# Optimization experiments

Hardware: AMD Instinct MI355X
Metric: run time of the kernel (lower is better)

## Reference

```python
import math
import jax, jax.numpy as jnp
import numpy as np

B = 2
TMAX = 1024
D = 1024
H = 16
DK = D // H
F = 4096
L = 2
CHUNK = 128
LEFT = 128
RIGHT = 32
EPS = 1e-5


def _build_mask(t_max, chunk, left, right):
    """Replicates EmformerEncoder.create_mask with audio_lens == t_max.
    Returns bool [T, T] where True = masked (disallowed), T = total_right + t_max."""
    num_chunks = math.ceil(t_max / chunk)
    ub = (num_chunks - 1) * right
    body = np.zeros((t_max, t_max), np.float32)
    mleft = np.zeros((t_max, ub), np.float32)
    mdiag = np.zeros((ub, ub), np.float32)
    mright = np.zeros((ub, t_max), np.float32)
    right_indexes = []
    for i in range(num_chunks):
        left_off = max(chunk * i - left, 0)
        start = chunk * i
        end = min(chunk * (i + 1), t_max)
        body[start:end, left_off:end] = 1
        if i == num_chunks - 1:
            break
        rem = t_max - (end + right)
        trl = right if rem >= 0 else t_max - end
        ri = len(right_indexes)
        mleft[start:start + chunk, ri:ri + trl] = 1
        mdiag[ri:ri + trl, ri:ri + trl] = 1
        mright[ri:ri + trl, left_off:end] = 1
        right_indexes += list(range(end, end + trl))
    rs = len(right_indexes)
    mleft = mleft[:, :rs]
    mdiag = mdiag[:rs, :rs]
    mright = mright[:rs, :]
    top = np.concatenate([mdiag, mright], axis=-1)
    bot = np.concatenate([mleft, body], axis=-1)
    m = np.concatenate([top, bot], axis=0)
    return m == 0  # True where attention is NOT allowed


def setup_inputs() -> dict:
    key = jax.random.key(0)
    ks = jax.random.split(key, 8)
    mask2d = _build_mask(TMAX, CHUNK, LEFT, RIGHT)  # [T, T]
    T = mask2d.shape[0]  # 1248
    w = lambda k, shape: jax.random.normal(k, shape, jnp.float32) * 0.02
    inp = {
        "input": jax.random.normal(ks[0], (B, T, D), jnp.float32),
        "ln_in_scale": jnp.ones((L, D), jnp.float32),
        "ln_in_bias": jnp.zeros((L, D), jnp.float32),
        "Wq": w(ks[1], (L, D, D)), "bq": jnp.zeros((L, D), jnp.float32),
        "Wk": w(ks[2], (L, D, D)), "bk": jnp.zeros((L, D), jnp.float32),
        "Wv": w(ks[3], (L, D, D)), "bv": jnp.zeros((L, D), jnp.float32),
        "ln1_scale": jnp.ones((L, D), jnp.float32),
        "ln1_bias": jnp.zeros((L, D), jnp.float32),
        "W1": w(ks[4], (L, D, F)), "b1": jnp.zeros((L, F), jnp.float32),
        "W2": w(ks[5], (L, F, D)), "b2": jnp.zeros((L, D), jnp.float32),
        "ln2_scale": jnp.ones((L, D), jnp.float32),
        "ln2_bias": jnp.zeros((L, D), jnp.float32),
        "mask": jnp.asarray(np.broadcast_to(mask2d[None, None], (B, 1, T, T)).copy()),
    }
    return inp


def _ln(x, scale, bias):
    m = jnp.mean(x, axis=-1, keepdims=True)
    v = jnp.mean(jnp.square(x - m), axis=-1, keepdims=True)
    return (x - m) * jax.lax.rsqrt(v + EPS) * scale + bias


def reference(input, ln_in_scale, ln_in_bias, Wq, bq, Wk, bk, Wv, bv,
              ln1_scale, ln1_bias, W1, b1, W2, b2, ln2_scale, ln2_bias, mask):
    x = input
    Bx, T, _ = x.shape
    scale = 1.0 / math.sqrt(DK)
    for l in range(L):
        h = _ln(x, ln_in_scale[l], ln_in_bias[l])  # pre-LN input (also residual base)
        q = (h @ Wq[l] + bq[l]).reshape(Bx, T, H, DK)
        k = (h @ Wk[l] + bk[l]).reshape(Bx, T, H, DK)
        v = (h @ Wv[l] + bv[l]).reshape(Bx, T, H, DK)
        scores = jnp.einsum('bqhd,bkhd->bhqk', q, k) * scale  # [B,H,T,T]
        scores = jnp.where(mask, -jnp.inf, scores)
        probs = jax.nn.softmax(scores, axis=-1)
        probs = jnp.where(mask, 0.0, probs)  # dropout_attn=0 -> identity
        o = jnp.einsum('bhqk,bkhd->bqhd', probs, v).reshape(Bx, T, D)
        attn_out = o + h
        y = _ln(attn_out, ln1_scale[l], ln1_bias[l])
        y = y @ W1[l] + b1[l]          # note: no activation in original code
        y = y @ W2[l] + b2[l] + attn_out
        x = _ln(y, ln2_scale[l], ln2_bias[l])
    return x
```

## Files before the change

### kernel.cpp

```cpp
#include <hip/hip_runtime.h>
#include <stdint.h>

typedef __attribute__((ext_vector_type(8))) short short8;
typedef __attribute__((ext_vector_type(4))) float f32x4;
typedef __attribute__((ext_vector_type(2))) _Float16 half2_t;

#define DEV __device__ __forceinline__

DEV float bits2f(uint32_t u){ union{uint32_t u;float f;}v; v.u=u; return v.f; }
DEV float bf_lo(uint32_t w){ return bits2f(w<<16); }
DEV float bf_hi(uint32_t w){ return bits2f(w & 0xffff0000u); }
DEV float bf1(uint16_t s){ return bits2f(((uint32_t)s)<<16); }
DEV uint16_t f2bf(float f){ union{float f;uint32_t u;}v; v.f=f; uint32_t u=v.u;
  return (uint16_t)((u + 0x7fffu + ((u>>16)&1u))>>16); }
DEV uint16_t f2h(float a){ union{_Float16 h; uint16_t u;}v; v.h=(_Float16)a; return v.u; }
DEV float h2f(uint16_t s){ union{uint16_t u; _Float16 h;}v; v.u=s; return (float)v.h; }

DEV float ldval(const float* p, size_t i){ return p[i]; }
DEV float ldval(const uint16_t* p, size_t i){ return bf1(p[i]); }
DEV void stval(float* p, size_t i, float v){ p[i]=v; }
DEV void stval(uint16_t* p, size_t i, float v){ p[i]=f2bf(v); }

DEV void async16(const void* g, void* l){
#if __has_builtin(__builtin_amdgcn_global_load_lds)
  __builtin_amdgcn_global_load_lds((const __attribute__((address_space(1))) void*)g,
                                   (__attribute__((address_space(3))) void*)l, 16, 0, 0);
#else
  int lane = threadIdx.x & 63;
  *(uint4*)((char*)l + lane*16) = *(const uint4*)((const char*)g);
#endif
}

template<int TM, int TN, bool SPLIT>
__global__ __launch_bounds__(256) void gemm_t(
    const uint16_t* __restrict__ A, const uint16_t* __restrict__ Bt,
    const float* __restrict__ bias, void* __restrict__ Cout,
    int N, int K, int kchunk) {
  __shared__ uint16_t sA[3][TM*32];
  __shared__ uint16_t sB[3][TN*32];
  const int lin = blockIdx.y*gridDim.x + blockIdx.x;
  const int q8 = (gridDim.x*gridDim.y) >> 3;
  const int swz = (lin & 7)*q8 + (lin >> 3);
  const int mt_ = swz % gridDim.y, nt_ = swz / gridDim.y;
  const int m0 = mt_*TM, n0 = nt_*TN;
  const int kb = SPLIT ? blockIdx.z*kchunk : 0;
  const int kend = SPLIT ? kb + kchunk : K;
  const int tid = threadIdx.x, wid = tid>>6, lane = tid&63;
  constexpr int WM = TM/2, MT = WM/16;
  constexpr int WN = TN/2, NT = WN/16;
  const int wm = (wid&1)*WM, wn = (wid>>1)*WN;
  f32x4 acc[MT][NT];
  #pragma unroll
  for (int a=0;a<MT;a++)
    #pragma unroll
    for (int b=0;b<NT;b++) acc[a][b] = (f32x4){0.f,0.f,0.f,0.f};
  const int lrow = lane>>2;
  const int lcol = (((lane&3) ^ ((lrow>>1)&3)))*8;
  const int fr = lane&15, fc = lane>>4;
  const int rsw = (fc ^ ((fr>>1)&3))*8;

  auto stage = [&](int buf, int k0) {
    #pragma unroll
    for (int j = 0; j < TM/64; ++j) {
      int r0 = wid*(TM/4) + j*16;
      async16(A + (size_t)(m0+r0+lrow)*K + k0 + lcol, &sA[buf][r0*32]);
    }
    #pragma unroll
    for (int j = 0; j < TN/64; ++j) {
      int r0 = wid*(TN/4) + j*16;
      async16(Bt + (size_t)(n0+r0+lrow)*K + k0 + lcol, &sB[buf][r0*32]);
    }
  };

  const int niter = (kend - kb) >> 5;
  stage(0, kb);
  if (niter > 1) stage(1, kb + 32);
  int cur = 0;
  for (int it = 0; it < niter; ++it) {
    if (it+1 < niter) asm volatile("s_waitcnt vmcnt(4)" ::: "memory");
    else              asm volatile("s_waitcnt vmcnt(0)" ::: "memory");
    __builtin_amdgcn_s_barrier();
    __builtin_amdgcn_sched_barrier(0);
    if (it+2 < niter) {
      int b2 = cur+2; if (b2>=3) b2-=3;
      stage(b2, kb + (it+2)*32);
    }
    short8 af[MT], bfv[NT];
    #pragma unroll
    for (int t=0;t<MT;t++) af[t] = *(const short8*)&sA[cur][(wm + t*16 + fr)*32 + rsw];
    #pragma unroll
    for (int t=0;t<NT;t++) bfv[t] = *(const short8*)&sB[cur][(wn + t*16 + fr)*32 + rsw];
    #pragma unroll
    for (int mt=0;mt<MT;mt++)
      #pragma unroll
      for (int nt=0;nt<NT;nt++)
        acc[mt][nt] = __builtin_amdgcn_mfma_f32_16x16x32_bf16(af[mt], bfv[nt], acc[mt][nt], 0,0,0);
    if (++cur == 3) cur = 0;
  }
  const int cl = lane&15, rl = (lane>>4)*4;
  if (SPLIT) {
    float* Pz = (float*)Cout + (size_t)blockIdx.z*2560*N;
    #pragma unroll
    for (int nt=0;nt<NT;nt++) {
      int n = n0 + wn + nt*16 + cl;
      #pragma unroll
      for (int mt=0;mt<MT;mt++)
        #pragma unroll
        for (int r=0;r<4;r++)
          Pz[(size_t)(m0 + wm + mt*16 + rl + r)*N + n] = acc[mt][nt][r];
    }
  } else {
    uint16_t* C = (uint16_t*)Cout;
    #pragma unroll
    for (int nt=0;nt<NT;nt++) {
      int n = n0 + wn + nt*16 + cl;
      float bv = bias ? bias[n] : 0.f;
      #pragma unroll
      for (int mt=0;mt<MT;mt++)
        #pragma unroll
        for (int r=0;r<4;r++)
          C[(size_t)(m0 + wm + mt*16 + rl + r)*N + n] = f2bf(acc[mt][nt][r] + bv);
    }
  }
}

template<typename TI, typename TO>
DEV void ln_body(int row, int tid, const TI* x, const float* sc, const float* bi,
                 TO* out, float* red) {
  const size_t base = (size_t)row*1024 + tid*4;
  float v0=ldval(x,base), v1=ldval(x,base+1), v2=ldval(x,base+2), v3=ldval(x,base+3);
  float s = v0+v1+v2+v3;
  float sq = v0*v0+v1*v1+v2*v2+v3*v3;
  #pragma unroll
  for (int off=32; off; off>>=1){ s += __shfl_xor(s,off); sq += __shfl_xor(sq,off); }
  int wid=tid>>6, lane=tid&63;
  if (lane==0){ red[wid]=s; red[4+wid]=sq; }
  __syncthreads();
  s = red[0]+red[1]+red[2]+red[3]; sq = red[4]+red[5]+red[6]+red[7];
  float mean = s*(1.f/1024.f);
  float inv  = rsqrtf(sq*(1.f/1024.f) - mean*mean + 1e-5f);
  int c = tid*4;
  stval(out, base,   (v0-mean)*inv*sc[c]   + bi[c]);
  stval(out, base+1, (v1-mean)*inv*sc[c+1] + bi[c+1]);
  stval(out, base+2, (v2-mean)*inv*sc[c+2] + bi[c+2]);
  stval(out, base+3, (v3-mean)*inv*sc[c+3] + bi[c+3]);
}

template<typename TI, typename TO>
__global__ __launch_bounds__(256) void ln_k(const TI* __restrict__ x,
    const float* __restrict__ sc, const float* __restrict__ bi,
    TO* __restrict__ out) {
  __shared__ float red[8];
  ln_body<TI,TO>(blockIdx.x, threadIdx.x, x, sc, bi, out, red);
}

template<typename TO>
__global__ __launch_bounds__(256) void ln2_fused(const float* __restrict__ P,
    const float* __restrict__ b2, const uint16_t* __restrict__ resid,
    const float* __restrict__ sc, const float* __restrict__ bi,
    TO* __restrict__ out) {
  const int row = blockIdx.x, tid = threadIdx.x;
  const size_t base = (size_t)row*1024 + tid*4;
  float4 p0 = *(const float4*)(P + base);
  float4 p1 = *(const float4*)(P + (size_t)2560*1024 + base);
  int c = tid*4;
  float v0 = p0.x+p1.x+b2[c]  +bf1(resid[base]);
  float v1 = p0.y+p1.y+b2[c+1]+bf1(resid[base+1]);
  float v2 = p0.z+p1.z+b2[c+2]+bf1(resid[base+2]);
  float v3 = p0.w+p1.w+b2[c+3]+bf1(resid[base+3]);
  float s = v0+v1+v2+v3;
  float sq = v0*v0+v1*v1+v2*v2+v3*v3;
  #pragma unroll
  for (int off=32; off; off>>=1){ s += __shfl_xor(s,off); sq += __shfl_xor(sq,off); }
  __shared__ float red[8];
  int wid=tid>>6, lane=tid&63;
  if (lane==0){ red[wid]=s; red[4+wid]=sq; }
  __syncthreads();
  s = red[0]+red[1]+red[2]+red[3]; sq = red[4]+red[5]+red[6]+red[7];
  float mean = s*(1.f/1024.f);
  float inv  = rsqrtf(sq*(1.f/1024.f) - mean*mean + 1e-5f);
  stval(out, base,   (v0-mean)*inv*sc[c]   + bi[c]);
  stval(out, base+1, (v1-mean)*inv*sc[c+1] + bi[c+1]);
  stval(out, base+2, (v2-mean)*inv*sc[c+2] + bi[c+2]);
  stval(out, base+3, (v3-mean)*inv*sc[c+3] + bi[c+3]);
}

__global__ __launch_bounds__(256) void attn_fused(
    const uint32_t* __restrict__ qkv32, const uint16_t* __restrict__ hres,
    uint16_t* __restrict__ attn_out) {
  const int blk = blockIdx.x;
  const int qg = blk & 3, ci = (blk>>2)&7, hh = (blk>>5)&15, bb = blk>>9;
  const int sum_cnt = (ci<7)?32:0;
  const int bstart = (ci>=1)?128*(ci-1):0;
  const int bend = (ci==7)?1024:128*(ci+1);
  const int nk = sum_cnt + (bend - bstart);
  const int rowbase = bb*1248;
  const int tid = threadIdx.x, wid = tid>>6, lane = tid&63;
  const int fr = lane&15, fc = lane>>4;

  __shared__ uint16_t sm[30848];
  uint16_t* K16 = sm;
  uint32_t* KD  = (uint32_t*)sm;
  uint16_t* Q16 = sm + 20736;
  uint32_t* QD  = KD + 10368;
  uint16_t* SP16 = sm;
  uint16_t* V16 = sm + 11840;
  uint32_t* VD  = (uint32_t*)(sm + 11840);

  for (int idx = tid; idx < nk*32; idx += 256) {
    int j = idx>>5, d2 = idx&31;
    int tk = (j < sum_cnt) ? (32*ci + j) : (224 + bstart + (j - sum_cnt));
    KD[j*36 + d2] = qkv32[(size_t)(rowbase+tk)*1536 + 512 + hh*32 + d2];
  }
  for (int idx = tid; idx < 40*32; idx += 256) {
    int j = idx>>5, d2 = idx&31;
    int ql = qg*40 + j;
    int tq = (ql<32) ? (32*ci+ql) : (224+128*ci+ql-32);
    QD[j*36 + d2] = qkv32[(size_t)(rowbase+tq)*1536 + hh*32 + d2];
  }
  __syncthreads();

  const int n_mt = nk>>4;
  const int qoff[3] = {0,16,24};
  f32x4 accs[5][3];
  #pragma unroll
  for (int a=0;a<5;a++)
    #pragma unroll
    for (int b=0;b<3;b++) accs[a][b] = (f32x4){0.f,0.f,0.f,0.f};
  #pragma unroll
  for (int ks=0; ks<2; ++ks) {
    short8 bq_[3];
    #pragma unroll
    for (int nt=0;nt<3;nt++)
      bq_[nt] = *(const short8*)&Q16[(qoff[nt]+fr)*72 + ks*32 + fc*8];
    #pragma unroll
    for (int t=0;t<5;t++) {
      int mt = wid + 4*t;
      if (mt < n_mt) {
        short8 a_ = *(const short8*)&K16[(mt*16+fr)*72 + ks*32 + fc*8];
        #pragma unroll
        for (int nt=0;nt<3;nt++)
          accs[t][nt] = __builtin_amdgcn_mfma_f32_16x16x32_bf16(a_, bq_[nt], accs[t][nt], 0,0,0);
      }
    }
  }
  __syncthreads();

  #pragma unroll
  for (int t=0;t<5;t++) {
    int mt = wid + 4*t;
    if (mt < n_mt) {
      #pragma unroll
      for (int nt=0;nt<3;nt++) {
        int q = qoff[nt] + fr;
        #pragma unroll
        for (int r=0;r<4;r++)
          SP16[q*296 + mt*16 + fc*4 + r] = f2h(accs[t][nt][r]*0.125f);
      }
    }
  }
  for (int idx = tid; idx < nk*32; idx += 256) {
    int j = idx>>5, d2 = idx&31;
    int tk = (j < sum_cnt) ? (32*ci + j) : (224 + bstart + (j - sum_cnt));
    VD[j*33 + d2] = qkv32[(size_t)(rowbase+tk)*1536 + 1024 + hh*32 + d2];
  }
  __syncthreads();

  for (int i=0;i<10;i++) {
    int row = wid*10 + i;
    float v[5];
    #pragma unroll
    for (int g=0;g<5;g++){ int k=g*64+lane; v[g] = (k<nk) ? h2f(SP16[row*296+k]) : -1e30f; }
    float mx = fmaxf(fmaxf(fmaxf(v[0],v[1]),fmaxf(v[2],v[3])),v[4]);
    #pragma unroll
    for (int off=32; off; off>>=1) mx = fmaxf(mx, __shfl_xor(mx,off));
    float p[5], sum=0.f;
    #pragma unroll
    for (int g=0;g<5;g++){ p[g] = __expf(v[g]-mx); if (g*64+lane>=nk) p[g]=0.f; sum+=p[g]; }
    #pragma unroll
    for (int off=32; off; off>>=1) sum += __shfl_xor(sum,off);
    float inv = 1.f/sum;
    #pragma unroll
    for (int g=0;g<5;g++){ int k=g*64+lane; if (k<nk) SP16[row*296+k] = f2bf(p[g]*inv); }
  }
  __syncthreads();

  const int nkt = nk>>5;
  f32x4 acco[3];
  #pragma unroll
  for (int t=0;t<3;t++) acco[t] = (f32x4){0.f,0.f,0.f,0.f};
  const uint16_t* vcol = V16 + wid*16 + fr;
  for (int kt=0; kt<nkt; ++kt) {
    short8 bv_;
    #pragma unroll
    for (int j=0;j<8;j++) bv_[j] = (short)vcol[(kt*32 + fc*8 + j)*66];
    #pragma unroll
    for (int t=0;t<3;t++) {
      short8 a_ = *(const short8*)&SP16[(qoff[t]+fr)*296 + kt*32 + fc*8];
      acco[t] = __builtin_amdgcn_mfma_f32_16x16x32_bf16(a_, bv_, acco[t], 0,0,0);
    }
  }
  #pragma unroll
  for (int t=0;t<3;t++) {
    #pragma unroll
    for (int r=0;r<4;r++) {
      bool vq = true;
      if (ci==7 && qg==0 && (qoff[t]+fc*4+r)<32) vq = false;
      if (vq) {
        int qll = qg*40 + qoff[t] + fc*4 + r;
        int tq = (qll<32) ? (32*ci+qll) : (224+128*ci+qll-32);
        size_t addr = (size_t)(rowbase+tq)*1024 + hh*64 + wid*16 + fr;
        attn_out[addr] = f2bf(acco[t][r] + bf1(hres[addr]));
      }
    }
  }
}

__global__ void prep_k(const float* __restrict__ Wq, const float* __restrict__ Wk,
                       const float* __restrict__ Wv, const float* __restrict__ W1,
                       const float* __restrict__ W2, const float* __restrict__ bq,
                       const float* __restrict__ bk, const float* __restrict__ bv,
                       uint16_t* __restrict__ wt_qkv, uint16_t* __restrict__ wt_w1,
                       uint16_t* __restrict__ wt_w2, float* __restrict__ bqkv,
                       const void* __restrict__ lnx, int lnx_f32,
                       const float* __restrict__ lnsc, const float* __restrict__ lnbi,
                       uint16_t* __restrict__ lnout) {
  __shared__ float t[32][33];
  const int blk = blockIdx.x;
  const int tx = threadIdx.x, ty = threadIdx.y;
  if (blk >= 11276) {
    int row = blk - 11276;
    int tid = ty*32 + tx;
    float* red = &t[0][0];
    if (lnx_f32) ln_body<float,uint16_t>((int)row, tid, (const float*)lnx, lnsc, lnbi, lnout, red);
    else         ln_body<uint16_t,uint16_t>((int)row, tid, (const uint16_t*)lnx, lnsc, lnbi, lnout, red);
    return;
  }
  if (blk >= 11264) {
    int i = (blk-11264)*256 + ty*32 + tx;
    bqkv[i] = (i<1024) ? bq[i] : ((i<2048) ? bk[i-1024] : bv[i-2048]);
    return;
  }
  const float* src; uint16_t* dst; int R, C, c0, r0;
  if (blk < 3072) {
    int w = blk>>10, tt = blk&1023;
    src = (w==0)?Wq:((w==1)?Wk:Wv); dst = wt_qkv + (size_t)w*1048576;
    R = 1024; C = 1024; c0 = (tt&31)*32; r0 = (tt>>5)*32;
  } else if (blk < 7168) {
    int tt = blk-3072;
    src = W1; dst = wt_w1; R = 1024; C = 4096;
    c0 = (tt&127)*32; r0 = (tt>>7)*32;
  } else {
    int tt = blk-7168;
    src = W2; dst = wt_w2; R = 4096; C = 1024;
    c0 = (tt&31)*32; r0 = (tt>>5)*32;
  }
  #pragma unroll
  for (int i=0;i<4;i++) t[ty+8*i][tx] = src[(size_t)(r0+ty+8*i)*C + c0+tx];
  __syncthreads();
  #pragma unroll
  for (int i=0;i<4;i++) dst[(size_t)(c0+ty+8*i)*R + r0+tx] = f2bf(t[tx][ty+8*i]);
}

extern "C" void kernel_launch(void* const* d_in, const int* in_sizes, int n_in,
                              void* d_out, int out_size, void* d_ws, size_t ws_size,
                              hipStream_t stream) {
  const float* input  = (const float*)d_in[0];
  const float* lnin_s = (const float*)d_in[1];
  const float* lnin_b = (const float*)d_in[2];
  const float* Wq = (const float*)d_in[3];
  const float* bq = (const float*)d_in[4];
  const float* Wk = (const float*)d_in[5];
  const float* bk = (const float*)d_in[6];
  const float* Wv = (const float*)d_in[7];
  const float* bv = (const float*)d_in[8];
  const float* ln1_s = (const float*)d_in[9];
  const float* ln1_b = (const float*)d_in[10];
  const float* W1 = (const float*)d_in[11];
  const float* b1 = (const float*)d_in[12];
  const float* W2 = (const float*)d_in[13];
  const float* b2 = (const float*)d_in[14];
  const float* ln2_s = (const float*)d_in[15];
  const float* ln2_b = (const float*)d_in[16];

  char* ws = (char*)d_ws;
  uint16_t* wt_qkv = (uint16_t*)(ws + 0);
  uint16_t* wt_w1  = (uint16_t*)(ws + 6291456);
  uint16_t* wt_w2  = (uint16_t*)(ws + 14680064);
  float*    bqkv   = (float*)   (ws + 23068672);
  uint16_t* hbuf   = (uint16_t*)(ws + 23080960);
  uint16_t* qkvb   = (uint16_t*)(ws + 28323840);
  uint16_t* attnb  = (uint16_t*)(ws + 44052480);
  uint16_t* zbuf   = (uint16_t*)(ws + 49295360);
  float*    pbuf   = (float*)   (ws + 54538240);
  uint16_t* y1b    = hbuf;
  uint16_t* x1b    = zbuf;

  const uint16_t* xcur_bf = x1b;
  for (int l=0; l<2; ++l) {
    prep_k<<<13772, dim3(32,8), 0, stream>>>(Wq+(size_t)l*1048576, Wk+(size_t)l*1048576,
        Wv+(size_t)l*1048576, W1+(size_t)l*4194304, W2+(size_t)l*4194304,
        bq+l*1024, bk+l*1024, bv+l*1024, wt_qkv, wt_w1, wt_w2, bqkv,
        (l==0) ? (const void*)input : (const void*)xcur_bf, (l==0)?1:0,
        lnin_s+l*1024, lnin_b+l*1024, hbuf);

    gemm_t<128,128,false><<<dim3(24,20),256,0,stream>>>(hbuf, wt_qkv, bqkv, qkvb, 3072, 1024, 1024);
    attn_fused<<<1024,256,0,stream>>>((const uint32_t*)qkvb, hbuf, attnb);
    ln_k<uint16_t,uint16_t><<<2496,256,0,stream>>>(attnb, ln1_s+l*1024, ln1_b+l*1024, zbuf);
    gemm_t<128,128,false><<<dim3(32,20),256,0,stream>>>(zbuf, wt_w1, b1+l*4096, y1b, 4096, 1024, 1024);
    gemm_t<128,128,true><<<dim3(8,20,2),256,0,stream>>>(y1b, wt_w2, nullptr, pbuf, 1024, 4096, 2048);
    if (l==1) ln2_fused<float>   <<<2496,256,0,stream>>>(pbuf, b2+l*1024, attnb, ln2_s+l*1024, ln2_b+l*1024, (float*)d_out);
    else      ln2_fused<uint16_t><<<2496,256,0,stream>>>(pbuf, b2+l*1024, attnb, ln2_s+l*1024, ln2_b+l*1024, x1b);
  }
  (void)in_sizes; (void)n_in; (void)out_size; (void)ws_size;
}
```

Measured before the change: 510.0 us.

## Vectorize attention QKV loads, add setprio, retile W2 GEMM to 128x64

The attention kernel now loads K, Q and V rows from global memory as 16-byte vectors instead of 4-byte words. It raises wave priority around the MFMA loops with s_setprio. The split-K W2 GEMM switches to 128x64 tiles with twice as many column blocks to give more workgroups. The vmcnt wait count is now derived from loads per stage, which the smaller tile needs to stay correct. The changes aim to cut load instruction count and improve occupancy and load balance on the down-projection, at the cost of less reuse per tile.

```diff
diff --git a/kernel.cpp b/kernel.cpp
--- a/kernel.cpp
+++ b/kernel.cpp
@@ -8,8 +8,6 @@
 #define DEV __device__ __forceinline__
 
 DEV float bits2f(uint32_t u){ union{uint32_t u;float f;}v; v.u=u; return v.f; }
-DEV float bf_lo(uint32_t w){ return bits2f(w<<16); }
-DEV float bf_hi(uint32_t w){ return bits2f(w & 0xffff0000u); }
 DEV float bf1(uint16_t s){ return bits2f(((uint32_t)s)<<16); }
 DEV uint16_t f2bf(float f){ union{float f;uint32_t u;}v; v.f=f; uint32_t u=v.u;
   return (uint16_t)((u + 0x7fffu + ((u>>16)&1u))>>16); }
@@ -38,6 +36,7 @@
     int N, int K, int kchunk) {
   __shared__ uint16_t sA[3][TM*32];
   __shared__ uint16_t sB[3][TN*32];
+  constexpr int LPS = TM/64 + TN/64;
   const int lin = blockIdx.y*gridDim.x + blockIdx.x;
   const int q8 = (gridDim.x*gridDim.y) >> 3;
   const int swz = (lin & 7)*q8 + (lin >> 3);
@@ -77,8 +76,13 @@
   if (niter > 1) stage(1, kb + 32);
   int cur = 0;
   for (int it = 0; it < niter; ++it) {
-    if (it+1 < niter) asm volatile("s_waitcnt vmcnt(4)" ::: "memory");
-    else              asm volatile("s_waitcnt vmcnt(0)" ::: "memory");
+    if (it+1 < niter) {
+      if constexpr (LPS == 4)      asm volatile("s_waitcnt vmcnt(4)" ::: "memory");
+      else if constexpr (LPS == 3) asm volatile("s_waitcnt vmcnt(3)" ::: "memory");
+      else                         asm volatile("s_waitcnt vmcnt(2)" ::: "memory");
+    } else {
+      asm volatile("s_waitcnt vmcnt(0)" ::: "memory");
+    }
     __builtin_amdgcn_s_barrier();
     __builtin_amdgcn_sched_barrier(0);
     if (it+2 < niter) {
@@ -198,7 +202,7 @@
   const int tid = threadIdx.x, wid = tid>>6, lane = tid&63;
   const int fr = lane&15, fc = lane>>4;
 
-  __shared__ uint16_t sm[30848];
+  __shared__ __attribute__((aligned(16))) uint16_t sm[30848];
   uint16_t* K16 = sm;
   uint32_t* KD  = (uint32_t*)sm;
   uint16_t* Q16 = sm + 20736;
@@ -207,16 +211,18 @@
   uint16_t* V16 = sm + 11840;
   uint32_t* VD  = (uint32_t*)(sm + 11840);
 
-  for (int idx = tid; idx < nk*32; idx += 256) {
-    int j = idx>>5, d2 = idx&31;
+  for (int idx = tid; idx < nk*8; idx += 256) {
+    int j = idx>>3, q4 = idx&7;
     int tk = (j < sum_cnt) ? (32*ci + j) : (224 + bstart + (j - sum_cnt));
-    KD[j*36 + d2] = qkv32[(size_t)(rowbase+tk)*1536 + 512 + hh*32 + d2];
-  }
-  for (int idx = tid; idx < 40*32; idx += 256) {
-    int j = idx>>5, d2 = idx&31;
+    *(uint4*)&KD[j*36 + q4*4] =
+      *(const uint4*)&qkv32[(size_t)(rowbase+tk)*1536 + 512 + hh*32 + q4*4];
+  }
+  for (int idx = tid; idx < 40*8; idx += 256) {
+    int j = idx>>3, q4 = idx&7;
     int ql = qg*40 + j;
     int tq = (ql<32) ? (32*ci+ql) : (224+128*ci+ql-32);
-    QD[j*36 + d2] = qkv32[(size_t)(rowbase+tq)*1536 + hh*32 + d2];
+    *(uint4*)&QD[j*36 + q4*4] =
+      *(const uint4*)&qkv32[(size_t)(rowbase+tq)*1536 + hh*32 + q4*4];
   }
   __syncthreads();
 
@@ -227,6 +233,7 @@
   for (int a=0;a<5;a++)
     #pragma unroll
     for (int b=0;b<3;b++) accs[a][b] = (f32x4){0.f,0.f,0.f,0.f};
+  __builtin_amdgcn_s_setprio(1);
   #pragma unroll
   for (int ks=0; ks<2; ++ks) {
     short8 bq_[3];
@@ -244,6 +251,7 @@
       }
     }
   }
+  __builtin_amdgcn_s_setprio(0);
   __syncthreads();
 
   #pragma unroll
@@ -259,10 +267,12 @@
       }
     }
   }
-  for (int idx = tid; idx < nk*32; idx += 256) {
-    int j = idx>>5, d2 = idx&31;
+  for (int idx = tid; idx < nk*8; idx += 256) {
+    int j = idx>>3, q4 = idx&7;
     int tk = (j < sum_cnt) ? (32*ci + j) : (224 + bstart + (j - sum_cnt));
-    VD[j*33 + d2] = qkv32[(size_t)(rowbase+tk)*1536 + 1024 + hh*32 + d2];
+    uint4 w = *(const uint4*)&qkv32[(size_t)(rowbase+tk)*1536 + 1024 + hh*32 + q4*4];
+    uint32_t* dst = &VD[j*33 + q4*4];
+    dst[0]=w.x; dst[1]=w.y; dst[2]=w.z; dst[3]=w.w;
   }
   __syncthreads();
 
@@ -290,6 +300,7 @@
   #pragma unroll
   for (int t=0;t<3;t++) acco[t] = (f32x4){0.f,0.f,0.f,0.f};
   const uint16_t* vcol = V16 + wid*16 + fr;
+  __builtin_amdgcn_s_setprio(1);
   for (int kt=0; kt<nkt; ++kt) {
     short8 bv_;
     #pragma unroll
@@ -300,6 +311,7 @@
       acco[t] = __builtin_amdgcn_mfma_f32_16x16x32_bf16(a_, bv_, acco[t], 0,0,0);
     }
   }
+  __builtin_amdgcn_s_setprio(0);
   #pragma unroll
   for (int t=0;t<3;t++) {
     #pragma unroll
@@ -408,7 +420,7 @@
     attn_fused<<<1024,256,0,stream>>>((const uint32_t*)qkvb, hbuf, attnb);
     ln_k<uint16_t,uint16_t><<<2496,256,0,stream>>>(attnb, ln1_s+l*1024, ln1_b+l*1024, zbuf);
     gemm_t<128,128,false><<<dim3(32,20),256,0,stream>>>(zbuf, wt_w1, b1+l*4096, y1b, 4096, 1024, 1024);
-    gemm_t<128,128,true><<<dim3(8,20,2),256,0,stream>>>(y1b, wt_w2, nullptr, pbuf, 1024, 4096, 2048);
+    gemm_t<128,64,true><<<dim3(16,20,2),256,0,stream>>>(y1b, wt_w2, nullptr, pbuf, 1024, 4096, 2048);
     if (l==1) ln2_fused<float>   <<<2496,256,0,stream>>>(pbuf, b2+l*1024, attnb, ln2_s+l*1024, ln2_b+l*1024, (float*)d_out);
     else      ln2_fused<uint16_t><<<2496,256,0,stream>>>(pbuf, b2+l*1024, attnb, ln2_s+l*1024, ln2_b+l*1024, x1b);
   }
```

Result: faster. 487.3 us (-4.5%).
